# Performance work log

Hardware: AMD Instinct MI355X
Metric: run time of the kernel (lower is better)

## Reference

```python
import jax, jax.numpy as jnp
import numpy as np

P, N, M = 4, 8192, 8192

def setup_inputs() -> dict:
    key = jax.random.key(0)
    k1, k2, k3, k4, k5 = jax.random.split(key, 5)
    return {
        "camera_pts": jax.random.normal(k1, (P, N, 3), dtype=jnp.float32),
        "cad_pts": jax.random.normal(k2, (P, M, 3), dtype=jnp.float32),
        "part_weight": jax.random.uniform(k3, (P,), dtype=jnp.float32),
        "rot_quat": jax.random.normal(k4, (P, 4), dtype=jnp.float32),
        "tra": jax.random.normal(k5, (P, 3, 1), dtype=jnp.float32),
    }

def _quat_to_rot(q):
    # q: [P,4] in (w,x,y,z) order, normalized outside
    a, b, c, d = q[:, 0], q[:, 1], q[:, 2], q[:, 3]
    rows = jnp.stack([
        1 - 2*c*c - 2*d*d, 2*b*c - 2*a*d,     2*a*c + 2*b*d,
        2*b*c + 2*a*d,     1 - 2*b*b - 2*d*d, 2*c*d - 2*a*b,
        2*b*d - 2*a*c,     2*a*b + 2*c*d,     1 - 2*b*b - 2*c*c,
    ], axis=-1)  # [P,9]
    return rows.reshape(-1, 3, 3)

def _chamfer(x, y):
    # x: [N,4], y: [M,4] -> scalar bidirectional chamfer (Euclidean, not squared)
    x2 = jnp.sum(x * x, axis=-1)              # [N]
    y2 = jnp.sum(y * y, axis=-1)              # [M]
    d2 = x2[:, None] + y2[None, :] - 2.0 * (x @ y.T)
    dist = jnp.sqrt(jnp.clip(d2, 0.0))        # [N,M]
    return jnp.mean(jnp.min(dist, axis=1)) + jnp.mean(jnp.min(dist, axis=0))

def reference(camera_pts, cad_pts, part_weight, rot_quat, tra):
    q = rot_quat / jnp.linalg.norm(rot_quat, axis=1, keepdims=True)
    rot = _quat_to_rot(q)                                       # [P,3,3]
    top = jnp.concatenate([rot, tra], axis=2)                   # [P,3,4]
    bottom = jnp.broadcast_to(jnp.array([[[0.0, 0.0, 0.0, 1.0]]], dtype=rot.dtype), (rot.shape[0], 1, 4))
    transforms = jnp.concatenate([top, bottom], axis=1)         # [P,4,4]
    ones_cad = jnp.ones(cad_pts.shape[:-1] + (1,), dtype=cad_pts.dtype)
    ones_cam = jnp.ones(camera_pts.shape[:-1] + (1,), dtype=camera_pts.dtype)
    cad_h = jnp.concatenate([cad_pts, ones_cad], axis=-1)       # [P,M,4]
    cam_h = jnp.concatenate([camera_pts, ones_cam], axis=-1)    # [P,N,4]
    cad_base = jnp.einsum('pij,pmj->pmi', transforms, cad_h)    # [P,M,4]
    cd = jax.vmap(_chamfer)(cad_base, cam_h)                    # [P]
    all_objective = jnp.sum(part_weight * cd)
    return all_objective, jax.lax.stop_gradient(transforms)
```

## Files before the change

### kernel.cpp

```cpp
#include <hip/hip_runtime.h>
#include <math.h>

#define NP 4
#define NN 8192
#define NM 8192

#define AKV_OFF 0
#define BKV_OFF 262144
#define HA_OFF  524288
#define HB_OFF  557056
#define MINS_OFF 589824

typedef _Float16 half8 __attribute__((ext_vector_type(8)));
typedef float float4v __attribute__((ext_vector_type(4)));

__device__ inline void split16(float v, _Float16& h, _Float16& l) {
    h = (_Float16)v;
    l = (_Float16)(v - (float)h);
}

__device__ inline void make_transform(const float* __restrict__ quat,
                                      const float* __restrict__ tra,
                                      int p, float T[12]) {
    float q0 = quat[p * 4 + 0], q1 = quat[p * 4 + 1];
    float q2 = quat[p * 4 + 2], q3 = quat[p * 4 + 3];
    float inv = 1.0f / sqrtf(q0 * q0 + q1 * q1 + q2 * q2 + q3 * q3);
    float a = q0 * inv, b = q1 * inv, c = q2 * inv, d = q3 * inv;
    T[0] = 1.0f - 2.0f * c * c - 2.0f * d * d;
    T[1] = 2.0f * b * c - 2.0f * a * d;
    T[2] = 2.0f * a * c + 2.0f * b * d;
    T[3] = tra[p * 3 + 0];
    T[4] = 2.0f * b * c + 2.0f * a * d;
    T[5] = 1.0f - 2.0f * b * b - 2.0f * d * d;
    T[6] = 2.0f * c * d - 2.0f * a * b;
    T[7] = tra[p * 3 + 1];
    T[8] = 2.0f * b * d - 2.0f * a * c;
    T[9] = 2.0f * a * b + 2.0f * c * d;
    T[10] = 1.0f - 2.0f * b * b - 2.0f * c * c;
    T[11] = tra[p * 3 + 2];
}

__global__ __launch_bounds__(256) void prep_kernel(
    const float* __restrict__ cam, const float* __restrict__ cad,
    const float* __restrict__ quat, const float* __restrict__ tra,
    float* __restrict__ ws, float* __restrict__ out) {
    int idx = blockIdx.x * 256 + threadIdx.x;
    const float INF = __uint_as_float(0x7f800000u);

    if (idx < NP * NM) {
        int p = idx >> 13;
        float T[12];
        make_transform(quat, tra, p, T);
        float x = cad[idx * 3 + 0];
        float y = cad[idx * 3 + 1];
        float z = cad[idx * 3 + 2];
        float vx = fmaf(T[0], x, fmaf(T[1], y, fmaf(T[2], z, T[3])));
        float vy = fmaf(T[4], x, fmaf(T[5], y, fmaf(T[6], z, T[7])));
        float vz = fmaf(T[8], x, fmaf(T[9], y, fmaf(T[10], z, T[11])));
        ws[HA_OFF + idx] = 0.5f * (vx * vx + vy * vy + vz * vz);
        _Float16 hx, lx, hy, ly, hz, lz;
        split16(-vx, hx, lx);
        split16(-vy, hy, ly);
        split16(-vz, hz, lz);
        half8 k0 = {hx, hy, hz, lx, ly, lz, hx, hy};
        half8 k1 = {hz, (_Float16)0, (_Float16)0, (_Float16)0,
                    (_Float16)0, (_Float16)0, (_Float16)0, (_Float16)0};
        ((half8*)(ws + AKV_OFF))[idx * 2 + 0] = k0;
        ((half8*)(ws + AKV_OFF))[idx * 2 + 1] = k1;
    } else {
        int k = idx - NP * NM;
        float vx = cam[k * 3 + 0];
        float vy = cam[k * 3 + 1];
        float vz = cam[k * 3 + 2];
        ws[HB_OFF + k] = 0.5f * (vx * vx + vy * vy + vz * vz);
        _Float16 hx, lx, hy, ly, hz, lz;
        split16(vx, hx, lx);
        split16(vy, hy, ly);
        split16(vz, hz, lz);
        half8 k0 = {hx, hy, hz, hx, hy, hz, lx, ly};
        half8 k1 = {lz, (_Float16)0, (_Float16)0, (_Float16)0,
                    (_Float16)0, (_Float16)0, (_Float16)0, (_Float16)0};
        ((half8*)(ws + BKV_OFF))[k * 2 + 0] = k0;
        ((half8*)(ws + BKV_OFF))[k * 2 + 1] = k1;
    }
    ws[MINS_OFF + idx] = INF;

    if (idx < 64) {
        int p2 = idx >> 4;
        int r = (idx >> 2) & 3;
        int c = idx & 3;
        float T[12];
        make_transform(quat, tra, p2, T);
        float v;
        if (r == 3)
            v = (c == 3) ? 1.0f : 0.0f;
        else
            v = T[r * 4 + c];
        out[1 + idx] = v;
    } else if (idx == 64) {
        out[0] = 0.0f;
    }
}

__global__ __launch_bounds__(256)
__attribute__((amdgpu_waves_per_eu(4, 8)))
void chamfer_mfma(const float* __restrict__ ws, float* mins) {
    int tid = threadIdx.x;
    int lane = tid & 63;
    int w = tid >> 6;
    int quad = lane >> 4;
    int col = lane & 15;
    int p8 = blockIdx.z * 8192;
    int mb = blockIdx.x * 256;
    int nb = blockIdx.y * 512;
    const float INF = __uint_as_float(0x7f800000u);

    const half8* akv = (const half8*)(ws + AKV_OFF);
    const half8* bkv = (const half8*)(ws + BKV_OFF);
    const float* hap = ws + HA_OFF + p8;
    const float* hbp = ws + HB_OFF + p8;

    __shared__ float sMA[256];
    __shared__ float sMB[4 * 512];

    const half8 zf = {(_Float16)0, (_Float16)0, (_Float16)0, (_Float16)0,
                      (_Float16)0, (_Float16)0, (_Float16)0, (_Float16)0};

    int mw = mb + w * 64;
    half8 af[4];
    float4v haT[4];
    float4v minA[4];
#pragma unroll
    for (int i = 0; i < 4; ++i) {
        int m = mw + i * 16 + col;
        af[i] = (quad < 2) ? akv[(size_t)(p8 + m) * 2 + quad] : zf;
        haT[i] = *(const float4v*)(hap + mw + i * 16 + quad * 4);
        minA[i] = {INF, INF, INF, INF};
    }

    int n0 = nb + col;
    half8 bf = (quad < 2) ? bkv[(size_t)(p8 + n0) * 2 + quad] : zf;
    float hbs = hbp[n0];

#pragma unroll 4
    for (int j = 0; j < 32; ++j) {
        int jn = (j + 1) & 31;
        int n = nb + jn * 16 + col;
        half8 bf_n = (quad < 2) ? bkv[(size_t)(p8 + n) * 2 + quad] : zf;
        float hbs_n = hbp[n];

        float tb = INF;
#pragma unroll
        for (int i = 0; i < 4; ++i) {
            float4v c;
            c.x = haT[i].x + hbs;
            c.y = haT[i].y + hbs;
            c.z = haT[i].z + hbs;
            c.w = haT[i].w + hbs;
            c = __builtin_amdgcn_mfma_f32_16x16x32_f16(af[i], bf, c, 0, 0, 0);
            minA[i].x = fminf(minA[i].x, c.x);
            minA[i].y = fminf(minA[i].y, c.y);
            minA[i].z = fminf(minA[i].z, c.z);
            minA[i].w = fminf(minA[i].w, c.w);
            tb = fminf(tb, fminf(fminf(c.x, c.y), fminf(c.z, c.w)));
        }
        tb = fminf(tb, __shfl_xor(tb, 16));
        tb = fminf(tb, __shfl_xor(tb, 32));
        if (lane < 16) sMB[w * 512 + j * 16 + col] = tb;

        bf = bf_n;
        hbs = hbs_n;
    }

#pragma unroll
    for (int i = 0; i < 4; ++i) {
        float v0 = minA[i].x, v1 = minA[i].y, v2 = minA[i].z, v3 = minA[i].w;
#pragma unroll
        for (int s = 1; s < 16; s <<= 1) {
            v0 = fminf(v0, __shfl_xor(v0, s));
            v1 = fminf(v1, __shfl_xor(v1, s));
            v2 = fminf(v2, __shfl_xor(v2, s));
            v3 = fminf(v3, __shfl_xor(v3, s));
        }
        if (col == 0) {
            float4v pack = {v0, v1, v2, v3};
            *(float4v*)&sMA[w * 64 + i * 16 + quad * 4] = pack;
        }
    }
    __syncthreads();

    atomicMin((unsigned int*)&mins[p8 + mb + tid], __float_as_uint(sMA[tid]));
#pragma unroll
    for (int c = tid; c < 512; c += 256) {
        float v = fminf(fminf(sMB[c], sMB[512 + c]),
                        fminf(sMB[1024 + c], sMB[1536 + c]));
        atomicMin((unsigned int*)&mins[NP * NM + p8 + nb + c],
                  __float_as_uint(v));
    }
}

__global__ __launch_bounds__(256) void finalize_kernel(
    const float* __restrict__ ws, const float* __restrict__ w,
    float* __restrict__ out) {
    const float* vals = ws + MINS_OFF;
    int i = blockIdx.x * 256 + threadIdx.x;
    int tid = threadIdx.x;

    float wl[4] = {w[0], w[1], w[2], w[3]};

    int i2 = i + 32768;
    float acc = wl[(i >> 13) & 3] * sqrtf(fmaxf(2.0f * vals[i], 0.0f)) +
                wl[(i2 >> 13) & 3] * sqrtf(fmaxf(2.0f * vals[i2], 0.0f));

#pragma unroll
    for (int off = 32; off > 0; off >>= 1) acc += __shfl_down(acc, off, 64);

    __shared__ float wsum[4];
    if ((tid & 63) == 0) wsum[tid >> 6] = acc;
    __syncthreads();
    if (tid == 0) {
        float blocksum = (wsum[0] + wsum[1] + wsum[2] + wsum[3]) * (1.0f / 8192.0f);
        atomicAdd(out, blocksum);
    }
}

extern "C" void kernel_launch(void* const* d_in, const int* in_sizes, int n_in,
                              void* d_out, int out_size, void* d_ws, size_t ws_size,
                              hipStream_t stream) {
    const float* cam = (const float*)d_in[0];
    const float* cad = (const float*)d_in[1];
    const float* w = (const float*)d_in[2];
    const float* quat = (const float*)d_in[3];
    const float* tra = (const float*)d_in[4];
    float* out = (float*)d_out;
    float* ws = (float*)d_ws;

    prep_kernel<<<256, 256, 0, stream>>>(cam, cad, quat, tra, ws, out);

    dim3 grid(NM / 256, NN / 512, NP);
    chamfer_mfma<<<grid, 256, 0, stream>>>(ws, ws + MINS_OFF);

    finalize_kernel<<<128, 256, 0, stream>>>(ws, w, out);
}
```

Before: 124.8 us.

## Replace atomicMin reductions with per-block partial buffers and deepen B prefetch

The chamfer kernel no longer does atomicMin into a shared mins array. Each block instead writes its row and column partial minima to its own slice of a workspace buffer, and the finalize kernel min-reduces the 16 and 32 slices before the sqrt and weighted sum. This removes about 1.5M global atomics and the INF initialisation in the prep kernel, at the cost of extra partial-buffer traffic (roughly 6 MB read in finalize) and a larger workspace. The B-fragment prefetch in the inner loop also goes from one to two iterations ahead, to better hide load latency.

```diff
diff --git a/kernel.cpp b/kernel.cpp
--- a/kernel.cpp
+++ b/kernel.cpp
@@ -9,7 +9,8 @@
 #define BKV_OFF 262144
 #define HA_OFF  524288
 #define HB_OFF  557056
-#define MINS_OFF 589824
+#define PARTA_OFF 589824
+#define PARTB_OFF 1114112
 
 typedef _Float16 half8 __attribute__((ext_vector_type(8)));
 typedef float float4v __attribute__((ext_vector_type(4)));
@@ -45,7 +46,6 @@
     const float* __restrict__ quat, const float* __restrict__ tra,
     float* __restrict__ ws, float* __restrict__ out) {
     int idx = blockIdx.x * 256 + threadIdx.x;
-    const float INF = __uint_as_float(0x7f800000u);
 
     if (idx < NP * NM) {
         int p = idx >> 13;
@@ -83,7 +83,6 @@
         ((half8*)(ws + BKV_OFF))[k * 2 + 0] = k0;
         ((half8*)(ws + BKV_OFF))[k * 2 + 1] = k1;
     }
-    ws[MINS_OFF + idx] = INF;
 
     if (idx < 64) {
         int p2 = idx >> 4;
@@ -104,7 +103,7 @@
 
 __global__ __launch_bounds__(256)
 __attribute__((amdgpu_waves_per_eu(4, 8)))
-void chamfer_mfma(const float* __restrict__ ws, float* mins) {
+void chamfer_mfma(const float* __restrict__ ws, float* __restrict__ part) {
     int tid = threadIdx.x;
     int lane = tid & 63;
     int w = tid >> 6;
@@ -138,26 +137,29 @@
         minA[i] = {INF, INF, INF, INF};
     }
 
-    int n0 = nb + col;
-    half8 bf = (quad < 2) ? bkv[(size_t)(p8 + n0) * 2 + quad] : zf;
-    float hbs = hbp[n0];
+    int na = nb + col;
+    int nbv = nb + 16 + col;
+    half8 bf0 = (quad < 2) ? bkv[(size_t)(p8 + na) * 2 + quad] : zf;
+    float hb0 = hbp[na];
+    half8 bf1 = (quad < 2) ? bkv[(size_t)(p8 + nbv) * 2 + quad] : zf;
+    float hb1 = hbp[nbv];
 
 #pragma unroll 4
     for (int j = 0; j < 32; ++j) {
-        int jn = (j + 1) & 31;
+        int jn = (j + 2) & 31;
         int n = nb + jn * 16 + col;
-        half8 bf_n = (quad < 2) ? bkv[(size_t)(p8 + n) * 2 + quad] : zf;
-        float hbs_n = hbp[n];
+        half8 bf2 = (quad < 2) ? bkv[(size_t)(p8 + n) * 2 + quad] : zf;
+        float hb2 = hbp[n];
 
         float tb = INF;
 #pragma unroll
         for (int i = 0; i < 4; ++i) {
             float4v c;
-            c.x = haT[i].x + hbs;
-            c.y = haT[i].y + hbs;
-            c.z = haT[i].z + hbs;
-            c.w = haT[i].w + hbs;
-            c = __builtin_amdgcn_mfma_f32_16x16x32_f16(af[i], bf, c, 0, 0, 0);
+            c.x = haT[i].x + hb0;
+            c.y = haT[i].y + hb0;
+            c.z = haT[i].z + hb0;
+            c.w = haT[i].w + hb0;
+            c = __builtin_amdgcn_mfma_f32_16x16x32_f16(af[i], bf0, c, 0, 0, 0);
             minA[i].x = fminf(minA[i].x, c.x);
             minA[i].y = fminf(minA[i].y, c.y);
             minA[i].z = fminf(minA[i].z, c.z);
@@ -168,8 +170,8 @@
         tb = fminf(tb, __shfl_xor(tb, 32));
         if (lane < 16) sMB[w * 512 + j * 16 + col] = tb;
 
-        bf = bf_n;
-        hbs = hbs_n;
+        bf0 = bf1; hb0 = hb1;
+        bf1 = bf2; hb1 = hb2;
     }
 
 #pragma unroll
@@ -189,28 +191,35 @@
     }
     __syncthreads();
 
-    atomicMin((unsigned int*)&mins[p8 + mb + tid], __float_as_uint(sMA[tid]));
+    part[(size_t)(PARTA_OFF - PARTA_OFF) + (size_t)blockIdx.y * 32768 + p8 + mb + tid] = sMA[tid];
+    float* partB = part + (PARTB_OFF - PARTA_OFF);
 #pragma unroll
     for (int c = tid; c < 512; c += 256) {
         float v = fminf(fminf(sMB[c], sMB[512 + c]),
                         fminf(sMB[1024 + c], sMB[1536 + c]));
-        atomicMin((unsigned int*)&mins[NP * NM + p8 + nb + c],
-                  __float_as_uint(v));
+        partB[(size_t)blockIdx.x * 32768 + p8 + nb + c] = v;
     }
 }
 
 __global__ __launch_bounds__(256) void finalize_kernel(
     const float* __restrict__ ws, const float* __restrict__ w,
     float* __restrict__ out) {
-    const float* vals = ws + MINS_OFF;
+    const float* partA = ws + PARTA_OFF;
+    const float* partB = ws + PARTB_OFF;
     int i = blockIdx.x * 256 + threadIdx.x;
     int tid = threadIdx.x;
-
-    float wl[4] = {w[0], w[1], w[2], w[3]};
-
-    int i2 = i + 32768;
-    float acc = wl[(i >> 13) & 3] * sqrtf(fmaxf(2.0f * vals[i], 0.0f)) +
-                wl[(i2 >> 13) & 3] * sqrtf(fmaxf(2.0f * vals[i2], 0.0f));
+    const float INF = __uint_as_float(0x7f800000u);
+
+    float va = INF;
+#pragma unroll
+    for (int s = 0; s < 16; ++s) va = fminf(va, partA[s * 32768 + i]);
+    float vb = INF;
+#pragma unroll
+    for (int s = 0; s < 32; ++s) vb = fminf(vb, partB[s * 32768 + i]);
+
+    float wp = w[(i >> 13) & 3];
+    float acc = wp * (sqrtf(fmaxf(2.0f * va, 0.0f)) +
+                      sqrtf(fmaxf(2.0f * vb, 0.0f)));
 
 #pragma unroll
     for (int off = 32; off > 0; off >>= 1) acc += __shfl_down(acc, off, 64);
@@ -238,7 +247,7 @@
     prep_kernel<<<256, 256, 0, stream>>>(cam, cad, quat, tra, ws, out);
 
     dim3 grid(NM / 256, NN / 512, NP);
-    chamfer_mfma<<<grid, 256, 0, stream>>>(ws, ws + MINS_OFF);
+    chamfer_mfma<<<grid, 256, 0, stream>>>(ws, ws + PARTA_OFF);
 
     finalize_kernel<<<128, 256, 0, stream>>>(ws, w, out);
 }
```

Result: slower. 148.5 us (+19.0%).
